# Optimization experiments

Measured on AMD Instinct MI355X. Metric: run time of the kernel, lower is better.

The kernel has to match this reference:

```python
import jax, jax.numpy as jnp
import numpy as np

N, F, FP, K = 4096, 512, 64, 8
ALPHA = 0.2  # leaky relu slope
NEG_INF = -1e16


def setup_inputs() -> dict:
    key = jax.random.key(0)
    k1, k2, k3, k4 = jax.random.split(key, 4)
    gain = np.sqrt(2.0 / (1.0 + ALPHA ** 2))
    node_matrix = jax.random.normal(k1, (N, F), dtype=jnp.float32)
    adjacency_matrix = jax.random.randint(k2, (N, N), 0, 2, dtype=jnp.int32)
    W = jax.random.normal(k3, (K, F, FP), dtype=jnp.float32) * (gain * np.sqrt(2.0 / (F + FP)))
    a = jax.random.normal(k4, (K, 2 * FP, 1), dtype=jnp.float32) * (gain * np.sqrt(2.0 / (2 * FP + 1)))
    return {"node_matrix": node_matrix, "adjacency_matrix": adjacency_matrix, "W": W, "a": a}


def reference(node_matrix, adjacency_matrix, W, a):
    # hidden_repr: [K, N, F']
    h = jnp.einsum('nf,kfp->knp', node_matrix, W)
    a_src = a[:, :FP, 0]   # applied to attended-to node j (first half -> row vector)
    a_dst = a[:, FP:, 0]   # applied to query node i (second half -> column vector)
    f1 = jnp.einsum('knp,kp->kn', h, a_src)  # [K, N] scores for j
    f2 = jnp.einsum('knp,kp->kn', h, a_dst)  # [K, N] scores for i
    # e[k, i, j] = LeakyReLU(f2[k, i] + f1[k, j])  -> [K, N, N]
    e = jax.nn.leaky_relu(f2[:, :, None] + f1[:, None, :], negative_slope=ALPHA)
    e = jnp.where(adjacency_matrix[None, :, :] > 0, e, NEG_INF)
    att = jax.nn.softmax(e, axis=-1)
    out = jnp.einsum('knm,kmp->knp', att, h)  # [K, N, F']
    # concat heads along feature dim -> [N, K*F']
    return jnp.transpose(out, (1, 0, 2)).reshape(N, K * FP)
```

## Files before the change

### kernel.cpp

```cpp
#include <hip/hip_runtime.h>

#define N 4096
#define F 512
#define FP 64
#define K 8
#define KFP 512
#define LOG2E 1.44269504088896f

#define BI 64
#define BJ 256
#define NTILE (N / BJ)
#define SMH 65536

typedef __attribute__((ext_vector_type(8))) short short8;
typedef __attribute__((ext_vector_type(4))) float f32x4;
typedef __attribute__((ext_vector_type(2))) float f32x2;

__device__ __forceinline__ unsigned short f2bs(float x) {
  union { __bf16 b; unsigned short u; } u;
  u.b = (__bf16)x;
  return u.u;
}

#if __has_builtin(__builtin_amdgcn_exp2f)
#define EXP2(x) __builtin_amdgcn_exp2f(x)
#else
#define EXP2(x) __expf((x) * 0.6931471805599453f)
#endif

__device__ __forceinline__ f32x2 pk_add(f32x2 a, f32x2 b) {
  f32x2 d;
  asm("v_pk_add_f32 %0, %1, %2" : "=v"(d) : "v"(a), "v"(b));
  return d;
}
__device__ __forceinline__ f32x2 pk_mul(f32x2 a, f32x2 b) {
  f32x2 d;
  asm("v_pk_mul_f32 %0, %1, %2" : "=v"(d) : "v"(a), "v"(b));
  return d;
}

__device__ __forceinline__ float mask_w(float w, unsigned mb, int off) {
  return __int_as_float(__float_as_int(w) & __builtin_amdgcn_sbfe((int)mb, off, 1));
}

#define GLOAD_LDS(src, dst) \
  __builtin_amdgcn_global_load_lds( \
      (const __attribute__((address_space(1))) void*)(src), \
      (__attribute__((address_space(3))) void*)(dst), 16, 0, 0)

__global__ __launch_bounds__(256) void prep_fused(const float* __restrict__ X,
                                                  unsigned short* __restrict__ Xb,
                                                  const float* __restrict__ W,
                                                  unsigned short* __restrict__ Wt) {
  __shared__ unsigned short WT16[64][66];
  const int t = threadIdx.x;
  if (blockIdx.x < 1024) {
    const int idx = (blockIdx.x * 256 + t) * 8;
    const float4 v0 = *reinterpret_cast<const float4*>(&X[idx]);
    const float4 v1 = *reinterpret_cast<const float4*>(&X[idx + 4]);
    unsigned short o[8] = {f2bs(v0.x), f2bs(v0.y), f2bs(v0.z), f2bs(v0.w),
                           f2bs(v1.x), f2bs(v1.y), f2bs(v1.z), f2bs(v1.w)};
    *reinterpret_cast<uint4*>(&Xb[idx]) = *reinterpret_cast<uint4*>(&o[0]);
    return;
  }
  const int bid = blockIdx.x - 1024;
  const int k = bid >> 3;
  const int f0 = (bid & 7) * 64;
#pragma unroll
  for (int j = 0; j < 16; j++) {
    const int idx = j * 256 + t;
    const int fl = idx >> 6, p = idx & 63;
    WT16[p][fl] = f2bs(W[(k * F + f0 + fl) * FP + p]);
  }
  __syncthreads();
  const int p = t >> 2, uc = t & 3;
  unsigned short tmp[16];
#pragma unroll
  for (int j = 0; j < 16; j++) tmp[j] = WT16[p][uc * 16 + j];
  unsigned short* dst = &Wt[(k * 64 + p) * F + f0 + uc * 16];
  *reinterpret_cast<uint4*>(dst)     = *reinterpret_cast<uint4*>(&tmp[0]);
  *reinterpret_cast<uint4*>(dst + 8) = *reinterpret_cast<uint4*>(&tmp[8]);
}

__global__ __launch_bounds__(256, 2) void gemm_h(
    const unsigned short* __restrict__ Xb, const unsigned short* __restrict__ Wt,
    const float* __restrict__ a, unsigned short* __restrict__ h_bT,
    float* __restrict__ f1, float* __restrict__ f2,
    const int* __restrict__ adj, unsigned long long* __restrict__ adjb) {
  __shared__ __align__(16) unsigned char AT[2][8192];
  __shared__ __align__(16) unsigned char BT[2][8192];
  __shared__ float F1L[2][64], F2L[2][64];

  const int t = threadIdx.x;
  const int k = blockIdx.x & 7;
  const int n0 = (blockIdx.x >> 3) * 64;
  const int wave = t >> 6, lane = t & 63;
  const int cg = wave >> 1, ng = wave & 1;
  const int col = lane & 15, kg = lane >> 4;
  const unsigned short* __restrict__ Wk = Wt + (size_t)k * 64 * F;

  f32x4 acc[2][2];
#pragma unroll
  for (int i = 0; i < 2; i++)
#pragma unroll
    for (int j = 0; j < 2; j++) acc[i][j] = (f32x4){0.f, 0.f, 0.f, 0.f};

  auto stage = [&](int tt, int buf) {
    const int f0 = tt * 64;
#pragma unroll
    for (int m = 0; m < 2; m++) {
      const int g = wave * 128 + m * 64 + lane;
      const int row = g >> 3, pu = g & 7;
      const int u = pu ^ (row & 7);
      GLOAD_LDS(Wk + (size_t)row * F + f0 + u * 8,
                AT[buf] + (wave * 128 + m * 64) * 16);
      GLOAD_LDS(Xb + (size_t)(n0 + row) * F + f0 + u * 8,
                BT[buf] + (wave * 128 + m * 64) * 16);
    }
  };

  auto compute = [&](int buf) {
#pragma unroll
    for (int ks = 0; ks < 2; ks++) {
      const int u0 = ks * 4 + kg;
      short8 af[2], bf[2];
#pragma unroll
      for (int i = 0; i < 2; i++) {
        const int rowA = cg * 32 + i * 16 + col;
        af[i] = *reinterpret_cast<const short8*>(
            AT[buf] + (rowA * 8 + (u0 ^ (rowA & 7))) * 16);
        const int rowB = ng * 32 + i * 16 + col;
        bf[i] = *reinterpret_cast<const short8*>(
            BT[buf] + (rowB * 8 + (u0 ^ (rowB & 7))) * 16);
      }
#pragma unroll
      for (int i = 0; i < 2; i++)
#pragma unroll
        for (int j = 0; j < 2; j++)
          acc[i][j] = __builtin_amdgcn_mfma_f32_16x16x32_bf16(af[i], bf[j], acc[i][j], 0, 0, 0);
    }
  };

  int adjv[16];
  const int wb_wave = blockIdx.x * 512 + wave * 128;
  auto adj_load = [&](int c) {
    const int* p = adj + (size_t)(wb_wave + c * 16) * 64 + lane;
#pragma unroll
    for (int x = 0; x < 16; x++) adjv[x] = p[x * 64];
  };
  auto adj_process = [&](int c) {
    unsigned long long ms[16];
#pragma unroll
    for (int x = 0; x < 16; x++) ms[x] = __ballot(adjv[x] > 0);
    if (lane == 0) {
#pragma unroll
      for (int x = 0; x < 16; x++) adjb[wb_wave + c * 16 + x] = ms[x];
    }
  };

  stage(0, 0);
  adj_load(0);
  for (int tt = 0; tt < F / 64; ++tt) {
    const int cur = tt & 1;
    __builtin_amdgcn_s_barrier();
    __builtin_amdgcn_sched_barrier(0);
    if (tt + 1 < F / 64) {
      stage(tt + 1, 1 - cur);
      asm volatile("s_waitcnt vmcnt(4)" ::: "memory");
    } else {
      asm volatile("s_waitcnt vmcnt(0)" ::: "memory");
    }
    __builtin_amdgcn_s_barrier();
    __builtin_amdgcn_sched_barrier(0);
    if (tt >= 1) {
      adj_process(tt - 1);
      adj_load(tt);
    }
    compute(cur);
  }
  asm volatile("s_waitcnt vmcnt(0)" ::: "memory");
  adj_process(7);

  float p1[2] = {0.f, 0.f}, p2[2] = {0.f, 0.f};
#pragma unroll
  for (int i = 0; i < 2; i++) {
#pragma unroll
    for (int r = 0; r < 4; r++) {
      const int p = cg * 32 + i * 16 + kg * 4 + r;
      const float as = a[k * 128 + p];
      const float ad = a[k * 128 + 64 + p];
#pragma unroll
      for (int j = 0; j < 2; j++) {
        const float v = acc[i][j][r];
        h_bT[(size_t)(k * 64 + p) * N + n0 + ng * 32 + j * 16 + col] = f2bs(v);
        p1[j] = fmaf(v, as, p1[j]);
        p2[j] = fmaf(v, ad, p2[j]);
      }
    }
  }
#pragma unroll
  for (int j = 0; j < 2; j++) {
    p1[j] += __shfl_xor(p1[j], 16); p1[j] += __shfl_xor(p1[j], 32);
    p2[j] += __shfl_xor(p2[j], 16); p2[j] += __shfl_xor(p2[j], 32);
    if (kg == 0) {
      F1L[cg][ng * 32 + j * 16 + col] = p1[j];
      F2L[cg][ng * 32 + j * 16 + col] = p2[j];
    }
  }
  __syncthreads();
  if (t < 64) {
    f1[k * N + n0 + t] = (F1L[0][t] + F1L[1][t]) * LOG2E;
    f2[k * N + n0 + t] = (F2L[0][t] + F2L[1][t]) * LOG2E;
  }
}

__global__ __launch_bounds__(512, 4) void attn_mfma(
    const unsigned short* __restrict__ h_bT, const float* __restrict__ f1,
    const float* __restrict__ f2, const unsigned long long* __restrict__ adjb,
    float* __restrict__ out) {
  __shared__ __align__(16) unsigned char SMEM[SMH + 2048 + 4096];
  __shared__ float DL[2][4][32];

  const int tid = threadIdx.x;
  const int k = blockIdx.x & 7;
  const int i0 = (blockIdx.x >> 3) * BI;
  const int wave = tid >> 6, lane = tid & 63;
  const int iq = wave >> 2;
  const int jq = wave & 3;
  const int col = lane & 15, kg = lane >> 4;

  const float* __restrict__ f1k = f1 + k * N;
  const unsigned char* __restrict__ hbb =
      (const unsigned char*)(h_bT + (size_t)k * 64 * N);

  const int rbase = i0 + iq * 32;
  const float f2r0 = f2[k * N + rbase + col];
  const float f2r1 = f2[k * N + rbase + 16 + col];
  const f32x2 f2r0_2 = {f2r0, f2r0};
  const f32x2 f2r1_2 = {f2r1, f2r1};
  const f32x2 c02 = {0.2f, 0.2f};

  f32x4 acc[2][4];
  f32x4 accden[2];
#pragma unroll
  for (int a = 0; a < 2; a++) {
    accden[a] = (f32x4){0.f, 0.f, 0.f, 0.f};
#pragma unroll
    for (int n = 0; n < 4; n++) acc[a][n] = (f32x4){0.f, 0.f, 0.f, 0.f};
  }
  short8 bones;
#pragma unroll
  for (int e = 0; e < 8; e++) bones[e] = (short)0x3F80;

  auto stage = [&](int tt, int buf) {
#pragma unroll
    for (int m = 0; m < 4; m++) {
      const int g = wave * 4 + m;
      const int row = g * 2 + (lane >> 5);
      const int pu = lane & 31;
      const int u = pu ^ (row & 15);
      GLOAD_LDS(hbb + (size_t)row * (N * 2) + tt * (BJ * 2) + u * 16,
                SMEM + buf * 32768 + g * 1024);
    }
    if (wave == 0) {
      GLOAD_LDS(f1k + tt * BJ + lane * 4, SMEM + SMH + buf * 1024);
#pragma unroll
      for (int m = 0; m < 2; m++) {
        const int g = m * 64 + lane;
        const int row = g >> 1, half = g & 1;
        GLOAD_LDS(adjb + (size_t)(i0 + row) * 64 + tt * 4 + half * 2,
                  SMEM + SMH + 2048 + buf * 2048 + m * 1024);
      }
    }
  };

  auto compute_tile = [&](int buf) {
    const unsigned long long* ADJ =
        (const unsigned long long*)(SMEM + SMH + 2048 + buf * 2048);
    const uint2 aw0 = *reinterpret_cast<const uint2*>(&ADJ[(iq * 32 + col) * 4 + jq]);
    const uint2 aw1 = *reinterpret_cast<const uint2*>(&ADJ[(iq * 32 + 16 + col) * 4 + jq]);
    const float* F1 = (const float*)(SMEM + SMH + buf * 1024);
#pragma unroll
    for (int ks = 0; ks < 2; ks++) {
      const int jl = jq * 64 + ks * 32 + kg * 8;
      const float4 fa = *reinterpret_cast<const float4*>(&F1[jl]);
      const float4 fb = *reinterpret_cast<const float4*>(&F1[jl + 4]);
      const unsigned m0 = ks ? aw0.y : aw0.x;
      const unsigned m1 = ks ? aw1.y : aw1.x;

      short8 bfrag[4];
#pragma unroll
      for (int n = 0; n < 4; n++) {
        const int row_b = n * 16 + col;
        const int u = jq * 8 + ks * 4 + kg;
        const int pu = u ^ col;
        bfrag[n] = *reinterpret_cast<const short8*>(
            SMEM + buf * 32768 + row_b * 512 + pu * 16);
      }

      const f32x2 prs[4] = {{fa.x, fa.y}, {fa.z, fa.w}, {fb.x, fb.y}, {fb.z, fb.w}};
      union { unsigned u[4]; short8 s; } A0, A1;
#pragma unroll
      for (int e2 = 0; e2 < 4; e2++) {
        const f32x2 t0 = pk_add(prs[e2], f2r0_2);
        const f32x2 t1 = pk_add(prs[e2], f2r1_2);
        const f32x2 u0 = pk_mul(t0, c02);
        const f32x2 u1 = pk_mul(t1, c02);
        float w0a = EXP2(fmaxf(t0.x, u0.x));
        float w0b = EXP2(fmaxf(t0.y, u0.y));
        float w1a = EXP2(fmaxf(t1.x, u1.x));
        float w1b = EXP2(fmaxf(t1.y, u1.y));
        const int ob = kg * 8 + 2 * e2;
        w0a = mask_w(w0a, m0, ob);     w0b = mask_w(w0b, m0, ob + 1);
        w1a = mask_w(w1a, m1, ob);     w1b = mask_w(w1b, m1, ob + 1);
        asm("v_cvt_pk_bf16_f32 %0, %1, %2" : "=v"(A0.u[e2]) : "v"(w0a), "v"(w0b));
        asm("v_cvt_pk_bf16_f32 %0, %1, %2" : "=v"(A1.u[e2]) : "v"(w1a), "v"(w1b));
      }

      __builtin_amdgcn_s_setprio(1);
      accden[0] = __builtin_amdgcn_mfma_f32_16x16x32_bf16(A0.s, bones, accden[0], 0, 0, 0);
      accden[1] = __builtin_amdgcn_mfma_f32_16x16x32_bf16(A1.s, bones, accden[1], 0, 0, 0);
#pragma unroll
      for (int n = 0; n < 4; n++) {
        acc[0][n] = __builtin_amdgcn_mfma_f32_16x16x32_bf16(A0.s, bfrag[n], acc[0][n], 0, 0, 0);
        acc[1][n] = __builtin_amdgcn_mfma_f32_16x16x32_bf16(A1.s, bfrag[n], acc[1][n], 0, 0, 0);
      }
      __builtin_amdgcn_s_setprio(0);
    }
  };

  stage(0, 0);
  for (int t = 0; t < NTILE; ++t) {
    const int cur = t & 1;
    __builtin_amdgcn_s_barrier();
    __builtin_amdgcn_sched_barrier(0);
    if (t + 1 < NTILE) {
      stage(t + 1, 1 - cur);
      if (wave == 0) asm volatile("s_waitcnt vmcnt(7)" ::: "memory");
      else           asm volatile("s_waitcnt vmcnt(4)" ::: "memory");
    } else {
      asm volatile("s_waitcnt vmcnt(0)" ::: "memory");
    }
    __builtin_amdgcn_s_barrier();
    __builtin_amdgcn_sched_barrier(0);
    compute_tile(cur);
  }
  __syncthreads();

  float* CL = (float*)SMEM;
  if (jq != 0) {
#pragma unroll
    for (int a = 0; a < 2; a++) {
#pragma unroll
      for (int n = 0; n < 4; n++)
#pragma unroll
        for (int r = 0; r < 4; r++)
          CL[((iq * 3 + (jq - 1)) * 32 + a * 16 + kg * 4 + r) * 66 + n * 16 + col] =
              acc[a][n][r];
      if (col == 0)
#pragma unroll
        for (int r = 0; r < 4; r++) DL[iq][jq][a * 16 + kg * 4 + r] = accden[a][r];
    }
  } else {
#pragma unroll
    for (int a = 0; a < 2; a++)
      if (col == 0)
#pragma unroll
        for (int r = 0; r < 4; r++) DL[iq][0][a * 16 + kg * 4 + r] = accden[a][r];
  }
  __syncthreads();
  if (jq == 0) {
#pragma unroll
    for (int a = 0; a < 2; a++) {
#pragma unroll
      for (int r = 0; r < 4; r++) {
        const int il = a * 16 + kg * 4 + r;
        const float den = DL[iq][0][il] + DL[iq][1][il] + DL[iq][2][il] + DL[iq][3][il];
        const float rinv = 1.f / den;
#pragma unroll
        for (int n = 0; n < 4; n++) {
          float v = acc[a][n][r];
          v += CL[((iq * 3 + 0) * 32 + il) * 66 + n * 16 + col];
          v += CL[((iq * 3 + 1) * 32 + il) * 66 + n * 16 + col];
          v += CL[((iq * 3 + 2) * 32 + il) * 66 + n * 16 + col];
          out[(size_t)(i0 + iq * 32 + il) * KFP + k * 64 + n * 16 + col] = v * rinv;
        }
      }
    }
  }
}

extern "C" void kernel_launch(void* const* d_in, const int* in_sizes, int n_in,
                              void* d_out, int out_size, void* d_ws, size_t ws_size,
                              hipStream_t stream) {
  const float* X   = (const float*)d_in[0];
  const int*   adj = (const int*)d_in[1];
  const float* W   = (const float*)d_in[2];
  const float* a   = (const float*)d_in[3];
  float* out = (float*)d_out;

  char* ws = (char*)d_ws;
  unsigned short* h_bT = (unsigned short*)(ws);
  float* f1  = (float*)(ws + 4194304);
  float* f2  = (float*)(ws + 4325376);
  unsigned long long* adjb = (unsigned long long*)(ws + 4456448);
  unsigned short* Wt = (unsigned short*)(ws + 6553600);
  unsigned short* Xb = (unsigned short*)d_out;

  hipLaunchKernelGGL(prep_fused, dim3(1024 + K * (F / 64)), dim3(256), 0, stream,
                     X, Xb, W, Wt);
  hipLaunchKernelGGL(gemm_h, dim3(K * (N / 64)), dim3(256), 0, stream,
                     Xb, Wt, a, h_bT, f1, f2, adj, adjb);
  hipLaunchKernelGGL(attn_mfma, dim3((N / BI) * K), dim3(512), 0, stream,
                     h_bT, f1, f2, adjb, out);
}
```

Measured before the change: 79.48 us.

## Drop LDS staging in attention kernel, read h and adjacency directly from global

The attention kernel no longer double-buffers tiles of h, f1 and adjacency bits into LDS with async global-to-LDS loads and barriers. Instead, each of four waves handles its own quarter of the j range for a 32-row block and loads B fragments, f1 and mask words straight from global memory or cache. The block shrinks from 512 to 256 threads and the grid doubles. This removes the barrier and LDS traffic but loses reuse of h across row groups, roughly doubling global and L2 reads of h, and exposes memory latency with no explicit prefetch.

```diff
diff --git a/kernel.cpp b/kernel.cpp
--- a/kernel.cpp
+++ b/kernel.cpp
@@ -6,11 +6,6 @@
 #define K 8
 #define KFP 512
 #define LOG2E 1.44269504088896f
-
-#define BI 64
-#define BJ 256
-#define NTILE (N / BJ)
-#define SMH 65536
 
 typedef __attribute__((ext_vector_type(8))) short short8;
 typedef __attribute__((ext_vector_type(4))) float f32x4;
@@ -214,31 +209,29 @@
   }
 }
 
-__global__ __launch_bounds__(512, 4) void attn_mfma(
+__global__ __launch_bounds__(256, 4) void attn_mfma(
     const unsigned short* __restrict__ h_bT, const float* __restrict__ f1,
     const float* __restrict__ f2, const unsigned long long* __restrict__ adjb,
     float* __restrict__ out) {
-  __shared__ __align__(16) unsigned char SMEM[SMH + 2048 + 4096];
-  __shared__ float DL[2][4][32];
+  __shared__ float CL[3 * 32 * 66];
+  __shared__ float DL[4][32];
 
   const int tid = threadIdx.x;
   const int k = blockIdx.x & 7;
-  const int i0 = (blockIdx.x >> 3) * BI;
-  const int wave = tid >> 6, lane = tid & 63;
-  const int iq = wave >> 2;
-  const int jq = wave & 3;
+  const int i0 = (blockIdx.x >> 3) * 32;
+  const int jq = tid >> 6, lane = tid & 63;
   const int col = lane & 15, kg = lane >> 4;
 
   const float* __restrict__ f1k = f1 + k * N;
-  const unsigned char* __restrict__ hbb =
-      (const unsigned char*)(h_bT + (size_t)k * 64 * N);
-
-  const int rbase = i0 + iq * 32;
-  const float f2r0 = f2[k * N + rbase + col];
-  const float f2r1 = f2[k * N + rbase + 16 + col];
+  const unsigned short* __restrict__ hk = h_bT + (size_t)k * 64 * N;
+
+  const float f2r0 = f2[k * N + i0 + col];
+  const float f2r1 = f2[k * N + i0 + 16 + col];
   const f32x2 f2r0_2 = {f2r0, f2r0};
   const f32x2 f2r1_2 = {f2r1, f2r1};
   const f32x2 c02 = {0.2f, 0.2f};
+  const unsigned long long* __restrict__ ar0 = adjb + (size_t)(i0 + col) * 64;
+  const unsigned long long* __restrict__ ar1 = adjb + (size_t)(i0 + 16 + col) * 64;
 
   f32x4 acc[2][4];
   f32x4 accden[2];
@@ -252,51 +245,23 @@
 #pragma unroll
   for (int e = 0; e < 8; e++) bones[e] = (short)0x3F80;
 
-  auto stage = [&](int tt, int buf) {
-#pragma unroll
-    for (int m = 0; m < 4; m++) {
-      const int g = wave * 4 + m;
-      const int row = g * 2 + (lane >> 5);
-      const int pu = lane & 31;
-      const int u = pu ^ (row & 15);
-      GLOAD_LDS(hbb + (size_t)row * (N * 2) + tt * (BJ * 2) + u * 16,
-                SMEM + buf * 32768 + g * 1024);
-    }
-    if (wave == 0) {
-      GLOAD_LDS(f1k + tt * BJ + lane * 4, SMEM + SMH + buf * 1024);
-#pragma unroll
-      for (int m = 0; m < 2; m++) {
-        const int g = m * 64 + lane;
-        const int row = g >> 1, half = g & 1;
-        GLOAD_LDS(adjb + (size_t)(i0 + row) * 64 + tt * 4 + half * 2,
-                  SMEM + SMH + 2048 + buf * 2048 + m * 1024);
-      }
-    }
-  };
-
-  auto compute_tile = [&](int buf) {
-    const unsigned long long* ADJ =
-        (const unsigned long long*)(SMEM + SMH + 2048 + buf * 2048);
-    const uint2 aw0 = *reinterpret_cast<const uint2*>(&ADJ[(iq * 32 + col) * 4 + jq]);
-    const uint2 aw1 = *reinterpret_cast<const uint2*>(&ADJ[(iq * 32 + 16 + col) * 4 + jq]);
-    const float* F1 = (const float*)(SMEM + SMH + buf * 1024);
+  for (int jg = 0; jg < 16; ++jg) {
+    const int j0 = jq * 1024 + jg * 64;
+    const uint2 aw0 = *reinterpret_cast<const uint2*>(ar0 + (j0 >> 6));
+    const uint2 aw1 = *reinterpret_cast<const uint2*>(ar1 + (j0 >> 6));
 #pragma unroll
     for (int ks = 0; ks < 2; ks++) {
-      const int jl = jq * 64 + ks * 32 + kg * 8;
-      const float4 fa = *reinterpret_cast<const float4*>(&F1[jl]);
-      const float4 fb = *reinterpret_cast<const float4*>(&F1[jl + 4]);
+      const int jb = j0 + ks * 32 + kg * 8;
+      const float4 fa = *reinterpret_cast<const float4*>(&f1k[jb]);
+      const float4 fb = *reinterpret_cast<const float4*>(&f1k[jb + 4]);
       const unsigned m0 = ks ? aw0.y : aw0.x;
       const unsigned m1 = ks ? aw1.y : aw1.x;
 
       short8 bfrag[4];
 #pragma unroll
-      for (int n = 0; n < 4; n++) {
-        const int row_b = n * 16 + col;
-        const int u = jq * 8 + ks * 4 + kg;
-        const int pu = u ^ col;
+      for (int n = 0; n < 4; n++)
         bfrag[n] = *reinterpret_cast<const short8*>(
-            SMEM + buf * 32768 + row_b * 512 + pu * 16);
-      }
+            &hk[(size_t)(n * 16 + col) * N + jb]);
 
       const f32x2 prs[4] = {{fa.x, fa.y}, {fa.z, fa.w}, {fb.x, fb.y}, {fb.z, fb.w}};
       union { unsigned u[4]; short8 s; } A0, A1;
@@ -327,46 +292,22 @@
       }
       __builtin_amdgcn_s_setprio(0);
     }
-  };
-
-  stage(0, 0);
-  for (int t = 0; t < NTILE; ++t) {
-    const int cur = t & 1;
-    __builtin_amdgcn_s_barrier();
-    __builtin_amdgcn_sched_barrier(0);
-    if (t + 1 < NTILE) {
-      stage(t + 1, 1 - cur);
-      if (wave == 0) asm volatile("s_waitcnt vmcnt(7)" ::: "memory");
-      else           asm volatile("s_waitcnt vmcnt(4)" ::: "memory");
-    } else {
-      asm volatile("s_waitcnt vmcnt(0)" ::: "memory");
-    }
-    __builtin_amdgcn_s_barrier();
-    __builtin_amdgcn_sched_barrier(0);
-    compute_tile(cur);
-  }
-  __syncthreads();
-
-  float* CL = (float*)SMEM;
+  }
+
+  if (col == 0) {
+#pragma unroll
+    for (int a = 0; a < 2; a++)
+#pragma unroll
+      for (int r = 0; r < 4; r++) DL[jq][a * 16 + kg * 4 + r] = accden[a][r];
+  }
   if (jq != 0) {
 #pragma unroll
-    for (int a = 0; a < 2; a++) {
+    for (int a = 0; a < 2; a++)
 #pragma unroll
       for (int n = 0; n < 4; n++)
 #pragma unroll
         for (int r = 0; r < 4; r++)
-          CL[((iq * 3 + (jq - 1)) * 32 + a * 16 + kg * 4 + r) * 66 + n * 16 + col] =
-              acc[a][n][r];
-      if (col == 0)
-#pragma unroll
-        for (int r = 0; r < 4; r++) DL[iq][jq][a * 16 + kg * 4 + r] = accden[a][r];
-    }
-  } else {
-#pragma unroll
-    for (int a = 0; a < 2; a++)
-      if (col == 0)
-#pragma unroll
-        for (int r = 0; r < 4; r++) DL[iq][0][a * 16 + kg * 4 + r] = accden[a][r];
+          CL[((jq - 1) * 32 + a * 16 + kg * 4 + r) * 66 + n * 16 + col] = acc[a][n][r];
   }
   __syncthreads();
   if (jq == 0) {
@@ -375,15 +316,15 @@
 #pragma unroll
       for (int r = 0; r < 4; r++) {
         const int il = a * 16 + kg * 4 + r;
-        const float den = DL[iq][0][il] + DL[iq][1][il] + DL[iq][2][il] + DL[iq][3][il];
+        const float den = DL[0][il] + DL[1][il] + DL[2][il] + DL[3][il];
         const float rinv = 1.f / den;
 #pragma unroll
         for (int n = 0; n < 4; n++) {
           float v = acc[a][n][r];
-          v += CL[((iq * 3 + 0) * 32 + il) * 66 + n * 16 + col];
-          v += CL[((iq * 3 + 1) * 32 + il) * 66 + n * 16 + col];
-          v += CL[((iq * 3 + 2) * 32 + il) * 66 + n * 16 + col];
-          out[(size_t)(i0 + iq * 32 + il) * KFP + k * 64 + n * 16 + col] = v * rinv;
+          v += CL[(0 * 32 + il) * 66 + n * 16 + col];
+          v += CL[(1 * 32 + il) * 66 + n * 16 + col];
+          v += CL[(2 * 32 + il) * 66 + n * 16 + col];
+          out[(size_t)(i0 + il) * KFP + k * 64 + n * 16 + col] = v * rinv;
         }
       }
     }
@@ -411,6 +352,6 @@
                      X, Xb, W, Wt);
   hipLaunchKernelGGL(gemm_h, dim3(K * (N / 64)), dim3(256), 0, stream,
                      Xb, Wt, a, h_bT, f1, f2, adj, adjb);
-  hipLaunchKernelGGL(attn_mfma, dim3((N / BI) * K), dim3(512), 0, stream,
+  hipLaunchKernelGGL(attn_mfma, dim3((N / 32) * K), dim3(256), 0, stream,
                      h_bT, f1, f2, adjb, out);
 }
```

After: 111.2 us. 40.0% more time.
